# Kernel optimization log

Hardware: AMD Instinct MI355X
Metric: run time of the kernel (lower is better)

Reference implementation:

```python
import jax, jax.numpy as jnp
import numpy as np

F = 32  # node channels (both convs)


def ecc_conv(x, src, dst, e, fgn_w, fgn_b, root, bias):
    """Edge-conditioned conv: per-edge kernel from edge feats, gather-matmul-scatter."""
    n_nodes = x.shape[0]
    n_edges = e.shape[0]
    f_in = x.shape[1]
    # filter-generating network: (E, S) -> (E, F_in*F_out) -> (E, F_in, F_out)
    kernels = (e @ fgn_w + fgn_b).reshape(n_edges, f_in, F)
    # gather source node feats, per-edge matmul
    messages = jnp.einsum('ef,efo->eo', x[src], kernels)
    # scatter-sum to target nodes
    agg = jax.ops.segment_sum(messages, dst, num_segments=n_nodes)
    return jax.nn.relu(agg + x @ root + bias)


def setup_inputs() -> dict:
    key = jax.random.key(0)
    ks = jax.random.split(key, 12)
    N, E, S = 50000, 200000, 16
    s = 0.05  # small init scale to keep activations bounded through relu
    return {
        'x': jax.random.normal(ks[0], (N, F), jnp.float32),
        'e': jax.random.normal(ks[1], (E, S), jnp.float32),
        'src': jax.random.randint(ks[2], (E,), 0, N, jnp.int32),
        'dst': jax.random.randint(ks[3], (E,), 0, N, jnp.int32),
        'fgn_w1': jax.random.normal(ks[4], (S, F * F), jnp.float32) * s,
        'fgn_b1': jnp.zeros((F * F,), jnp.float32),
        'root1': jax.random.normal(ks[5], (F, F), jnp.float32) * s,
        'bias1': jnp.zeros((F,), jnp.float32),
        'fgn_w2': jax.random.normal(ks[6], (S, F * F), jnp.float32) * s,
        'fgn_b2': jnp.zeros((F * F,), jnp.float32),
        'root2': jax.random.normal(ks[7], (F, F), jnp.float32) * s,
        'bias2': jnp.zeros((F,), jnp.float32),
        'dense_w': jax.random.normal(ks[8], (F, 1), jnp.float32) * s,
        'dense_b': jnp.zeros((1,), jnp.float32),
    }


def reference(x, e, src, dst, fgn_w1, fgn_b1, root1, bias1,
              fgn_w2, fgn_b2, root2, bias2, dense_w, dense_b):
    h = ecc_conv(x, src, dst, e, fgn_w1, fgn_b1, root1, bias1)
    h = ecc_conv(h, src, dst, e, fgn_w2, fgn_b2, root2, bias2)
    pooled = jnp.sum(h, axis=0)          # global sum pool over nodes -> (F,)
    return pooled @ dense_w + dense_b    # (1,)
```

## Files before the change

kernel.cpp:

```cpp
#include <hip/hip_runtime.h>
#include <hip/hip_bf16.h>
#include <hip/hip_fp16.h>

#define F 32
#define S 16

typedef short v8s __attribute__((ext_vector_type(8)));
typedef _Float16 v8h __attribute__((ext_vector_type(8)));
typedef float v4f __attribute__((ext_vector_type(4)));

__device__ __forceinline__ float bf_lo(unsigned u) { return __uint_as_float(u << 16); }
__device__ __forceinline__ float bf_hi(unsigned u) { return __uint_as_float(u & 0xffff0000u); }
__device__ __forceinline__ unsigned short f2bf(float f) {
    __hip_bfloat16 h = __float2bfloat16(f);
    return *(unsigned short*)&h;
}
__device__ __forceinline__ unsigned short f2h(float f) {
    __half h = __float2half(f);
    return *(unsigned short*)&h;
}
__device__ __forceinline__ unsigned pack2(float a, float b) {
    __hip_bfloat162 h2 = __float22bfloat162_rn(make_float2(a, b));
    return *(unsigned*)&h2;
}
__device__ __forceinline__ unsigned pack2h(float a, float b) {
    __half2 h2 = __floats2half2_rn(a, b);
    return *(unsigned*)&h2;
}
static inline size_t align256(size_t b) { return (b + 255) & ~(size_t)255; }

__global__ __launch_bounds__(256) void prep_kernel(
    const float* __restrict__ w1, const float* __restrict__ b1, const float* __restrict__ r1,
    const float* __restrict__ w2, const float* __restrict__ b2, const float* __restrict__ r2,
    unsigned short* __restrict__ Wf1, unsigned short* __restrict__ Wf2,
    unsigned short* __restrict__ Rt1, unsigned short* __restrict__ Rt2,
    const int* __restrict__ dst, int* __restrict__ cnt,
    const float* __restrict__ x, unsigned short* __restrict__ x16,
    int N, int E, int eB)
{
    const int PER = 34 * 512 + 32 * 32;
    if (blockIdx.x < 144) {
        int tid = blockIdx.x * blockDim.x + threadIdx.x;
        if (tid >= 2 * PER) return;
        const int layer = tid / PER;
        const int rem   = tid % PER;
        const float* w = layer ? w2 : w1;
        const float* b = layer ? b2 : b1;
        const float* r = layer ? r2 : r1;
        if (rem < 34 * 512) {
            const int fi   = rem >> 9;
            const int rr   = rem & 511;
            const int lane = rr >> 3;
            const int j    = rr & 7;
            const int half = fi & 1;
            const int ck   = fi >> 1;
            const int o    = (half << 4) | (lane & 15);
            const int k    = ck * 32 + (lane >> 4) * 8 + j;
            const int s    = k >> 5, f = k & 31;
            const float v  = (s < S) ? w[s * (F * F) + f * F + o] : b[f * F + o];
            (layer ? Wf2 : Wf1)[rem] = f2h(v);
        } else {
            const int q = rem - 34 * 512;
            const int o = q >> 5, f = q & 31;
            (layer ? Rt2 : Rt1)[o * F + f] = f2bf(r[f * F + o]);
        }
    } else if (blockIdx.x < 144 + eB) {
        const int e = (blockIdx.x - 144) * blockDim.x + threadIdx.x;
        if (e < E) atomicAdd(&cnt[dst[e]], 1);
    } else {
        const int idx = (blockIdx.x - 144 - eB) * 256 + threadIdx.x;
        if (idx < N * 4) {
            const float4* p = (const float4*)(x + (size_t)idx * 8);
            float4 a = p[0], b = p[1];
            uint4 o;
            o.x = pack2h(a.x, a.y); o.y = pack2h(a.z, a.w);
            o.z = pack2h(b.x, b.y); o.w = pack2h(b.z, b.w);
            *(uint4*)(x16 + (size_t)idx * 8) = o;
        }
    }
}

__global__ __launch_bounds__(256) void scan_partial(
    const int* __restrict__ cnt, int* __restrict__ partial, int N)
{
    const int i = blockIdx.x * 256 + threadIdx.x;
    int v = (i < N) ? cnt[i] : 0;
    #pragma unroll
    for (int off = 32; off > 0; off >>= 1) v += __shfl_down(v, off, 64);
    __shared__ int wsum[4];
    const int wave = threadIdx.x >> 6, lane = threadIdx.x & 63;
    if (lane == 0) wsum[wave] = v;
    __syncthreads();
    if (threadIdx.x == 0)
        partial[blockIdx.x] = wsum[0] + wsum[1] + wsum[2] + wsum[3];
}

__global__ __launch_bounds__(256) void scan_final(
    const int* __restrict__ cnt, const int* __restrict__ partial,
    int* __restrict__ cursor, int* __restrict__ rowptr, int N)
{
    const int tid = threadIdx.x;
    __shared__ int pacc[256];
    int pre = 0;
    for (int j = tid; j < blockIdx.x; j += 256) pre += partial[j];
    pacc[tid] = pre;
    __syncthreads();
    #pragma unroll
    for (int off = 128; off > 0; off >>= 1) {
        if (tid < off) pacc[tid] += pacc[tid + off];
        __syncthreads();
    }
    const int blockPre = pacc[0];

    const int i = blockIdx.x * 256 + tid;
    const int v0 = (i < N) ? cnt[i] : 0;
    int v = v0;
    const int wave = tid >> 6, lane = tid & 63;
    #pragma unroll
    for (int off = 1; off < 64; off <<= 1) {
        int u = __shfl_up(v, off, 64);
        if (lane >= off) v += u;
    }
    __shared__ int wsum[4];
    if (lane == 63) wsum[wave] = v;
    __syncthreads();
    int woff = 0;
    for (int ww = 0; ww < 4; ++ww) woff += (ww < wave) ? wsum[ww] : 0;
    if (i < N) {
        const int excl = blockPre + woff + (v - v0);
        cursor[i] = excl;
        rowptr[i] = excl;
    }
}

__global__ __launch_bounds__(256) void scatter_kernel(
    const int* __restrict__ dst, int* __restrict__ cursor,
    int* __restrict__ perm, int E)
{
    int e = blockIdx.x * blockDim.x + threadIdx.x;
    if (e < E) {
        int p = atomicAdd(&cursor[dst[e]], 1);
        perm[p] = e;
    }
}

__global__ __launch_bounds__(256) void edge_msg(
    const unsigned short* __restrict__ x16,
    const float* __restrict__ ef,
    const int* __restrict__ src,
    const unsigned short* __restrict__ Wf,
    unsigned short* __restrict__ msg,
    int E)
{
    __shared__ v8h Wl[34 * 64];
    const int tid  = threadIdx.x;
    const int w    = tid >> 6;
    const int lane = tid & 63;
    const int lid  = lane & 15;
    const int quad = lane >> 4;

    {
        const uint4* s = (const uint4*)Wf;
        uint4* d = (uint4*)Wl;
        #pragma unroll
        for (int i = 0; i < 9; ++i) {
            const int idx = tid + 256 * i;
            if (idx < 2176) d[idx] = s[idx];
        }
    }
    __syncthreads();

    const int nTiles = (E + 15) >> 4;
    const int stride = gridDim.x * 4;
    int tile = blockIdx.x * 4 + w;
    if (tile >= nTiles) return;

    int  slot = tile * 16 + lid;
    bool live = (slot < E);
    int  s0   = live ? slot : 0;
    int  sn   = src[s0];
    v8h xh = *(const v8h*)(x16 + (size_t)sn * F + quad * 8);
    const float4* efv = (const float4*)(ef + (size_t)s0 * S);
    float4 c0 = efv[0], c1 = efv[1], c2 = efv[2], c3 = efv[3];

    while (true) {
        const int nextTile = tile + stride;
        v8h nxh;
        float4 nc0, nc1, nc2, nc3;
        bool nlive = false;
        if (nextTile < nTiles) {
            const int  ns_  = nextTile * 16 + lid;
            nlive = (ns_ < E);
            const int  ns0_ = nlive ? ns_ : 0;
            const int  nsn  = src[ns0_];
            nxh = *(const v8h*)(x16 + (size_t)nsn * F + quad * 8);
            const float4* nefv = (const float4*)(ef + (size_t)ns0_ * S);
            nc0 = nefv[0]; nc1 = nefv[1]; nc2 = nefv[2]; nc3 = nefv[3];
        }

        const float cs[S] = {c0.x, c0.y, c0.z, c0.w, c1.x, c1.y, c1.z, c1.w,
                             c2.x, c2.y, c2.z, c2.w, c3.x, c3.y, c3.z, c3.w};

        union { v8h h8; __half2 h2[4]; } xu;
        xu.h8 = xh;

        v4f acc0 = {0.f, 0.f, 0.f, 0.f};
        v4f acc1 = {0.f, 0.f, 0.f, 0.f};

        #pragma unroll
        for (int ck = 0; ck < S; ++ck) {
            const __half2 cc = __floats2half2_rn(cs[ck], cs[ck]);
            union { v8h h8; __half2 h2[4]; } fr;
            fr.h2[0] = __hmul2(cc, xu.h2[0]);
            fr.h2[1] = __hmul2(cc, xu.h2[1]);
            fr.h2[2] = __hmul2(cc, xu.h2[2]);
            fr.h2[3] = __hmul2(cc, xu.h2[3]);
            acc0 = __builtin_amdgcn_mfma_f32_16x16x32_f16(Wl[(2 * ck) * 64 + lane],     fr.h8, acc0, 0, 0, 0);
            acc1 = __builtin_amdgcn_mfma_f32_16x16x32_f16(Wl[(2 * ck + 1) * 64 + lane], fr.h8, acc1, 0, 0, 0);
        }
        acc0 = __builtin_amdgcn_mfma_f32_16x16x32_f16(Wl[32 * 64 + lane], xu.h8, acc0, 0, 0, 0);
        acc1 = __builtin_amdgcn_mfma_f32_16x16x32_f16(Wl[33 * 64 + lane], xu.h8, acc1, 0, 0, 0);

        if (live) {
            unsigned short* mp = msg + (size_t)slot * 32;
            uint2 p0, p1;
            p0.x = pack2(acc0[0], acc0[1]);
            p0.y = pack2(acc0[2], acc0[3]);
            p1.x = pack2(acc1[0], acc1[1]);
            p1.y = pack2(acc1[2], acc1[3]);
            *(uint2*)(mp + quad * 4)      = p0;
            *(uint2*)(mp + 16 + quad * 4) = p1;
        }

        if (nextTile >= nTiles) break;
        tile = nextTile;
        slot = tile * 16 + lid;
        live = nlive;
        xh = nxh;
        c0 = nc0; c1 = nc1; c2 = nc2; c3 = nc3;
    }
}

__global__ __launch_bounds__(256) void rootsum(
    const float* __restrict__ in,
    const unsigned short* __restrict__ msg,
    const int* __restrict__ rowptr,
    const int* __restrict__ cnt,
    const int* __restrict__ perm,
    const unsigned short* __restrict__ Rt,
    const float* __restrict__ bias,
    unsigned short* __restrict__ h16,
    int N)
{
    __shared__ float acc[64 * 33];
    __shared__ unsigned short As[64 * F];
    const int tid  = threadIdx.x;
    const int n0   = blockIdx.x * 64;
    const int w    = tid >> 6;
    const int lane = tid & 63;
    const int lid  = lane & 15;
    const int quad = lane >> 4;

    {
        const int nl = tid >> 2;
        const int kq = tid & 3;
        int n = n0 + nl; if (n > N - 1) n = N - 1;
        const float4* xp = (const float4*)(in + (size_t)n * F + kq * 8);
        float4 v0 = xp[0], v1 = xp[1];
        uint4 pk;
        pk.x = pack2(v0.x, v0.y);
        pk.y = pack2(v0.z, v0.w);
        pk.z = pack2(v1.x, v1.y);
        pk.w = pack2(v1.z, v1.w);
        const int slot = ((nl >> 4) * 4 + kq) * 16 + (nl & 15);
        *(uint4*)(As + slot * 8) = pk;
    }

    {
        const int nl = tid >> 2;
        const int oq = tid & 3;
        const int n  = n0 + nl;
        float a[8];
        #pragma unroll
        for (int j = 0; j < 8; ++j) a[j] = 0.f;
        if (n < N) {
            const int k0 = rowptr[n];
            const int k1 = k0 + cnt[n];
            for (int k = k0; k < k1; ++k) {
                const int e = perm[k];
                const uint4 q = *(const uint4*)(msg + (size_t)e * 32 + oq * 8);
                a[0] += bf_lo(q.x); a[1] += bf_hi(q.x);
                a[2] += bf_lo(q.y); a[3] += bf_hi(q.y);
                a[4] += bf_lo(q.z); a[5] += bf_hi(q.z);
                a[6] += bf_lo(q.w); a[7] += bf_hi(q.w);
            }
        }
        float* ap = acc + nl * 33 + oq * 8;
        #pragma unroll
        for (int j = 0; j < 8; ++j) ap[j] = a[j];
    }
    __syncthreads();

    const int jt  = w & 1;
    const int ns0 = (w >> 1) * 2;
    const v8s rf = *(const v8s*)(Rt + (size_t)(jt * 16 + lid) * F + quad * 8);
    const int o0 = jt * 16 + quad * 4;
    const float4 bs = *(const float4*)(bias + o0);

    #pragma unroll
    for (int i = 0; i < 2; ++i) {
        const int ns = ns0 + i;
        const v8s af = *(const v8s*)(As + (((ns * 4 + quad) * 16) + lid) * 8);
        v4f d = {0.f, 0.f, 0.f, 0.f};
        d = __builtin_amdgcn_mfma_f32_16x16x32_bf16(rf, af, d, 0, 0, 0);
        const int n = n0 + ns * 16 + lid;
        if (n < N) {
            const float* ap = acc + (ns * 16 + lid) * 33 + o0;
            float4 hv;
            hv.x = fmaxf(d[0] + ap[0] + bs.x, 0.f);
            hv.y = fmaxf(d[1] + ap[1] + bs.y, 0.f);
            hv.z = fmaxf(d[2] + ap[2] + bs.z, 0.f);
            hv.w = fmaxf(d[3] + ap[3] + bs.w, 0.f);
            uint2 hp;
            hp.x = pack2h(hv.x, hv.y);
            hp.y = pack2h(hv.z, hv.w);
            *(uint2*)(h16 + (size_t)n * F + o0) = hp;
        }
    }
}

__global__ __launch_bounds__(256) void rootsum_pool(
    const unsigned short* __restrict__ in16,
    const unsigned short* __restrict__ msg,
    const int* __restrict__ rowptr,
    const int* __restrict__ cnt,
    const int* __restrict__ perm,
    const unsigned short* __restrict__ Rt,
    const float* __restrict__ bias,
    float* __restrict__ bs,
    int N)
{
    __shared__ float acc[64 * 33];
    __shared__ unsigned short As[64 * F];
    __shared__ float poolbuf[4][16];
    const int tid  = threadIdx.x;
    const int n0   = blockIdx.x * 64;
    const int w    = tid >> 6;
    const int lane = tid & 63;
    const int lid  = lane & 15;
    const int quad = lane >> 4;

    {
        const int nl = tid >> 2;
        const int kq = tid & 3;
        int n = n0 + nl; if (n > N - 1) n = N - 1;
        const uint4 hv4 = *(const uint4*)(in16 + (size_t)n * F + kq * 8);
        const __half2* hh = (const __half2*)&hv4;
        float2 f0 = __half22float2(hh[0]);
        float2 f1 = __half22float2(hh[1]);
        float2 f2 = __half22float2(hh[2]);
        float2 f3 = __half22float2(hh[3]);
        uint4 pk;
        pk.x = pack2(f0.x, f0.y);
        pk.y = pack2(f1.x, f1.y);
        pk.z = pack2(f2.x, f2.y);
        pk.w = pack2(f3.x, f3.y);
        const int slot = ((nl >> 4) * 4 + kq) * 16 + (nl & 15);
        *(uint4*)(As + slot * 8) = pk;
    }

    {
        const int nl = tid >> 2;
        const int oq = tid & 3;
        const int n  = n0 + nl;
        float a[8];
        #pragma unroll
        for (int j = 0; j < 8; ++j) a[j] = 0.f;
        if (n < N) {
            const int k0 = rowptr[n];
            const int k1 = k0 + cnt[n];
            for (int k = k0; k < k1; ++k) {
                const int e = perm[k];
                const uint4 q = *(const uint4*)(msg + (size_t)e * 32 + oq * 8);
                a[0] += bf_lo(q.x); a[1] += bf_hi(q.x);
                a[2] += bf_lo(q.y); a[3] += bf_hi(q.y);
                a[4] += bf_lo(q.z); a[5] += bf_hi(q.z);
                a[6] += bf_lo(q.w); a[7] += bf_hi(q.w);
            }
        }
        float* ap = acc + nl * 33 + oq * 8;
        #pragma unroll
        for (int j = 0; j < 8; ++j) ap[j] = a[j];
    }
    __syncthreads();

    const int jt  = w & 1;
    const int ns0 = (w >> 1) * 2;
    const v8s rf = *(const v8s*)(Rt + (size_t)(jt * 16 + lid) * F + quad * 8);
    const int o0 = jt * 16 + quad * 4;
    const float4 bs4 = *(const float4*)(bias + o0);

    float psum[4] = {0.f, 0.f, 0.f, 0.f};

    #pragma unroll
    for (int i = 0; i < 2; ++i) {
        const int ns = ns0 + i;
        const v8s af = *(const v8s*)(As + (((ns * 4 + quad) * 16) + lid) * 8);
        v4f d = {0.f, 0.f, 0.f, 0.f};
        d = __builtin_amdgcn_mfma_f32_16x16x32_bf16(rf, af, d, 0, 0, 0);
        const int n = n0 + ns * 16 + lid;
        if (n < N) {
            const float* ap = acc + (ns * 16 + lid) * 33 + o0;
            psum[0] += fmaxf(d[0] + ap[0] + bs4.x, 0.f);
            psum[1] += fmaxf(d[1] + ap[1] + bs4.y, 0.f);
            psum[2] += fmaxf(d[2] + ap[2] + bs4.z, 0.f);
            psum[3] += fmaxf(d[3] + ap[3] + bs4.w, 0.f);
        }
    }

    #pragma unroll
    for (int m = 1; m < 16; m <<= 1) {
        psum[0] += __shfl_xor(psum[0], m, 64);
        psum[1] += __shfl_xor(psum[1], m, 64);
        psum[2] += __shfl_xor(psum[2], m, 64);
        psum[3] += __shfl_xor(psum[3], m, 64);
    }
    if (lid == 0) {
        #pragma unroll
        for (int j = 0; j < 4; ++j) poolbuf[w][quad * 4 + j] = psum[j];
    }
    __syncthreads();
    if (tid < 32) {
        const int jt2 = tid >> 4, idx = tid & 15;
        bs[(size_t)blockIdx.x * 32 + tid] = poolbuf[jt2][idx] + poolbuf[jt2 + 2][idx];
    }
}

__global__ __launch_bounds__(256) void final_fused(
    const float* __restrict__ bs, int nb,
    const float* __restrict__ dw, const float* __restrict__ db,
    float* __restrict__ out)
{
    const int ch = threadIdx.x & 31, g = threadIdx.x >> 5;
    float s = 0.f;
    for (int b = g; b < nb; b += 8) s += bs[(size_t)b * 32 + ch];
    __shared__ float red[256];
    red[threadIdx.x] = s;
    __syncthreads();
    if (threadIdx.x < 128) red[threadIdx.x] += red[threadIdx.x + 128];
    __syncthreads();
    if (threadIdx.x < 64) red[threadIdx.x] += red[threadIdx.x + 64];
    __syncthreads();
    if (threadIdx.x < 32) red[threadIdx.x] = (red[threadIdx.x] + red[threadIdx.x + 32]) * dw[threadIdx.x];
    __syncthreads();
    if (threadIdx.x == 0) {
        float t = 0.f;
        #pragma unroll
        for (int i = 0; i < 32; ++i) t += red[i];
        out[0] = t + db[0];
    }
}

__global__ __launch_bounds__(256) void pool_kernel(
    const float* __restrict__ h, float* __restrict__ pooled, int N)
{
    const int c = threadIdx.x & (F - 1);
    float p = 0.0f;
    for (int n = blockIdx.x * 8 + (threadIdx.x >> 5); n < N; n += gridDim.x * 8)
        p += h[(size_t)n * F + c];
    __shared__ float red[256];
    red[threadIdx.x] = p;
    __syncthreads();
    for (int off = 128; off >= F; off >>= 1) {
        if (threadIdx.x < off) red[threadIdx.x] += red[threadIdx.x + off];
        __syncthreads();
    }
    if (threadIdx.x < F) atomicAdd(&pooled[threadIdx.x], red[threadIdx.x]);
}

__global__ void final_kernel(
    const float* __restrict__ pooled, const float* __restrict__ dw,
    const float* __restrict__ db, float* __restrict__ out)
{
    const int o = threadIdx.x;
    float v = (o < F) ? pooled[o] * dw[o] : 0.0f;
    #pragma unroll
    for (int off = 32; off > 0; off >>= 1) v += __shfl_down(v, off, 64);
    if (o == 0) out[0] = v + db[0];
}

__global__ __launch_bounds__(256, 2) void ecc_edge_slow(
    const float* __restrict__ x, const float* __restrict__ ef,
    const int* __restrict__ src, const int* __restrict__ dst,
    const float* __restrict__ W, const float* __restrict__ B,
    float* __restrict__ agg, int E)
{
    const int tid = blockIdx.x * blockDim.x + threadIdx.x;
    const bool live = (tid < E);
    const int e = live ? tid : (E - 1);
    const int sn = src[e], dn = dst[e];
    float xr[F];
    const float4* xp = (const float4*)(x + (size_t)sn * F);
    #pragma unroll
    for (int i = 0; i < F / 4; ++i) {
        float4 v = xp[i];
        xr[4*i+0] = v.x; xr[4*i+1] = v.y; xr[4*i+2] = v.z; xr[4*i+3] = v.w;
    }
    float acc[F];
    #pragma unroll
    for (int o = 0; o < F; ++o) acc[o] = 0.0f;
    const float* erow = ef + (size_t)e * S;
    for (int s = 0; s < S; ++s) {
        const float es = erow[s];
        const float* Ws = W + s * (F * F);
        #pragma unroll
        for (int f = 0; f < F; ++f) {
            const float z = es * xr[f];
            #pragma unroll
            for (int o = 0; o < F; ++o) acc[o] = fmaf(z, Ws[f * F + o], acc[o]);
        }
    }
    #pragma unroll
    for (int f = 0; f < F; ++f) {
        const float xf = xr[f];
        #pragma unroll
        for (int o = 0; o < F; ++o) acc[o] = fmaf(xf, B[f * F + o], acc[o]);
    }
    if (live) {
        float* ap = agg + (size_t)dn * F;
        #pragma unroll
        for (int o = 0; o < F; ++o) atomicAdd(ap + o, acc[o]);
    }
}

__global__ __launch_bounds__(256) void ecc_node_slow(
    const float* __restrict__ xin, const float* __restrict__ root,
    const float* __restrict__ bias, float* __restrict__ h, int N)
{
    int t = blockIdx.x * blockDim.x + threadIdx.x;
    if (t >= N * F) return;
    const int n = t >> 5, o = t & (F - 1);
    const float* xrow = xin + (size_t)n * F;
    float v = h[t] + bias[o];
    #pragma unroll
    for (int f = 0; f < F; ++f) v = fmaf(xrow[f], root[f * F + o], v);
    h[t] = fmaxf(v, 0.0f);
}

extern "C" void kernel_launch(void* const* d_in, const int* in_sizes, int n_in,
                              void* d_out, int out_size, void* d_ws, size_t ws_size,
                              hipStream_t stream) {
    const float* x      = (const float*)d_in[0];
    const float* efeat  = (const float*)d_in[1];
    const int*   src    = (const int*)d_in[2];
    const int*   dst    = (const int*)d_in[3];
    const float* fgn_w1 = (const float*)d_in[4];
    const float* fgn_b1 = (const float*)d_in[5];
    const float* root1  = (const float*)d_in[6];
    const float* bias1  = (const float*)d_in[7];
    const float* fgn_w2 = (const float*)d_in[8];
    const float* fgn_b2 = (const float*)d_in[9];
    const float* root2  = (const float*)d_in[10];
    const float* bias2  = (const float*)d_in[11];
    const float* dense_w = (const float*)d_in[12];
    const float* dense_b = (const float*)d_in[13];

    const int N = in_sizes[0] / F;
    const int E = in_sizes[2];

    const int gridP    = (N + 255) / 256;
    const int rsBlocks = (N + 63) / 64;

    const size_t pooledB = 256;
    const size_t cntB    = align256((size_t)N * 4);
    const size_t rowB    = align256((size_t)N * 4);
    const size_t curB    = align256((size_t)N * 4);
    const size_t partB   = align256((size_t)gridP * 4);
    const size_t permB   = align256((size_t)E * 4);
    const size_t efsB    = align256((size_t)E * S * 4);
    const size_t srcsB   = align256((size_t)E * 4);
    const size_t msgB    = align256((size_t)E * 32 * 2);
    const size_t hB      = (size_t)N * F * 4;
    const size_t wfB     = align256((size_t)34 * 512 * 2);
    const size_t rtB     = align256((size_t)32 * 32 * 2);
    const size_t x16B    = align256((size_t)N * F * 2);

    const size_t offCnt  = pooledB;
    const size_t offRow  = offCnt + cntB;
    const size_t offCur  = offRow + rowB;
    const size_t offPart = offCur + curB;
    const size_t offPerm = offPart + partB;
    const size_t offEfs  = offPerm + permB;
    const size_t offSrcs = offEfs + efsB;
    const size_t offMsg  = offSrcs + srcsB;
    const size_t offH1   = offMsg + msgB;
    const size_t offH2   = offH1 + hB;
    const size_t offW1   = offH2 + hB;
    const size_t offW2   = offW1 + wfB;
    const size_t offR1   = offW2 + wfB;
    const size_t offR2   = offR1 + rtB;
    const size_t need    = offR2 + rtB;

    const int eB         = (E + 255) / 256;
    const int nodeBlocks = (N * F + 255) / 256;

    if (ws_size >= need && efsB >= 2 * x16B) {
        int* cnt     = (int*)((char*)d_ws + offCnt);
        int* rowptr  = (int*)((char*)d_ws + offRow);
        int* cursor  = (int*)((char*)d_ws + offCur);
        int* partial = (int*)((char*)d_ws + offPart);
        int* perm    = (int*)((char*)d_ws + offPerm);
        unsigned short* x16 = (unsigned short*)((char*)d_ws + offEfs);
        unsigned short* h16 = (unsigned short*)((char*)d_ws + offEfs + x16B);
        unsigned short* msg = (unsigned short*)((char*)d_ws + offMsg);
        float* bsum  = (float*)((char*)d_ws + offH2);
        unsigned short* Wf1 = (unsigned short*)((char*)d_ws + offW1);
        unsigned short* Wf2 = (unsigned short*)((char*)d_ws + offW2);
        unsigned short* Rt1 = (unsigned short*)((char*)d_ws + offR1);
        unsigned short* Rt2 = (unsigned short*)((char*)d_ws + offR2);

        hipMemsetAsync(d_ws, 0, pooledB + cntB, stream);

        const int xcB = (N * 4 + 255) / 256;
        prep_kernel<<<144 + eB + xcB, 256, 0, stream>>>(
            fgn_w1, fgn_b1, root1, fgn_w2, fgn_b2, root2,
            Wf1, Wf2, Rt1, Rt2, dst, cnt, x, x16, N, E, eB);

        scan_partial  <<<gridP, 256, 0, stream>>>(cnt, partial, N);
        scan_final    <<<gridP, 256, 0, stream>>>(cnt, partial, cursor, rowptr, N);
        scatter_kernel<<<eB, 256, 0, stream>>>(dst, cursor, perm, E);

        const int nTiles = (E + 15) / 16;
        int edgeBlocks = (nTiles + 3) / 4;
        if (edgeBlocks > 1024) edgeBlocks = 1024;

        edge_msg<<<edgeBlocks, 256, 0, stream>>>(x16, efeat, src, Wf1, msg, E);
        rootsum <<<rsBlocks, 256, 0, stream>>>(x, msg, rowptr, cnt, perm, Rt1, bias1, h16, N);

        edge_msg    <<<edgeBlocks, 256, 0, stream>>>(h16, efeat, src, Wf2, msg, E);
        rootsum_pool<<<rsBlocks, 256, 0, stream>>>(h16, msg, rowptr, cnt, perm, Rt2, bias2, bsum, N);

        final_fused<<<1, 256, 0, stream>>>(bsum, rsBlocks, dense_w, dense_b, (float*)d_out);
    } else {
        float* agg1   = (float*)d_ws;
        float* agg2   = agg1 + (size_t)N * F;
        float* pooled = agg2 + (size_t)N * F;
        hipMemsetAsync(d_ws, 0, (2 * (size_t)N * F + F) * sizeof(float), stream);
        ecc_edge_slow<<<eB, 256, 0, stream>>>(x, efeat, src, dst, fgn_w1, fgn_b1, agg1, E);
        ecc_node_slow<<<nodeBlocks, 256, 0, stream>>>(x, root1, bias1, agg1, N);
        ecc_edge_slow<<<eB, 256, 0, stream>>>(agg1, efeat, src, dst, fgn_w2, fgn_b2, agg2, E);
        ecc_node_slow<<<nodeBlocks, 256, 0, stream>>>(agg1, root2, bias2, agg2, N);
        pool_kernel <<<512, 256, 0, stream>>>(agg2, pooled, N);
        final_kernel<<<1, 64, 0, stream>>>(pooled, dense_w, dense_b, (float*)d_out);
    }
}
```

Baseline: 192.8 us.

## Write edge messages directly in destination-sorted order via inverse permutation

The scatter kernel now records, for each edge, its position in the destination-sorted order, and edge_msg writes each message straight to that sorted slot. The rootsum kernels then read messages contiguously by CSR index, which drops the perm indirection and the random 64-byte gathers. In exchange the message writes from edge_msg become scattered rather than coalesced, and each edge tile does one extra index load.

```diff
diff --git a/kernel.cpp b/kernel.cpp
--- a/kernel.cpp
+++ b/kernel.cpp
@@ -135,12 +135,12 @@
 
 __global__ __launch_bounds__(256) void scatter_kernel(
     const int* __restrict__ dst, int* __restrict__ cursor,
-    int* __restrict__ perm, int E)
+    int* __restrict__ inv, int E)
 {
     int e = blockIdx.x * blockDim.x + threadIdx.x;
     if (e < E) {
         int p = atomicAdd(&cursor[dst[e]], 1);
-        perm[p] = e;
+        inv[e] = p;
     }
 }
 
@@ -148,6 +148,7 @@
     const unsigned short* __restrict__ x16,
     const float* __restrict__ ef,
     const int* __restrict__ src,
+    const int* __restrict__ inv,
     const unsigned short* __restrict__ Wf,
     unsigned short* __restrict__ msg,
     int E)
@@ -179,6 +180,7 @@
     bool live = (slot < E);
     int  s0   = live ? slot : 0;
     int  sn   = src[s0];
+    int  iv   = inv[s0];
     v8h xh = *(const v8h*)(x16 + (size_t)sn * F + quad * 8);
     const float4* efv = (const float4*)(ef + (size_t)s0 * S);
     float4 c0 = efv[0], c1 = efv[1], c2 = efv[2], c3 = efv[3];
@@ -187,12 +189,14 @@
         const int nextTile = tile + stride;
         v8h nxh;
         float4 nc0, nc1, nc2, nc3;
+        int niv = 0;
         bool nlive = false;
         if (nextTile < nTiles) {
             const int  ns_  = nextTile * 16 + lid;
             nlive = (ns_ < E);
             const int  ns0_ = nlive ? ns_ : 0;
             const int  nsn  = src[ns0_];
+            niv = inv[ns0_];
             nxh = *(const v8h*)(x16 + (size_t)nsn * F + quad * 8);
             const float4* nefv = (const float4*)(ef + (size_t)ns0_ * S);
             nc0 = nefv[0]; nc1 = nefv[1]; nc2 = nefv[2]; nc3 = nefv[3];
@@ -222,7 +226,7 @@
         acc1 = __builtin_amdgcn_mfma_f32_16x16x32_f16(Wl[33 * 64 + lane], xu.h8, acc1, 0, 0, 0);
 
         if (live) {
-            unsigned short* mp = msg + (size_t)slot * 32;
+            unsigned short* mp = msg + (size_t)iv * 32;
             uint2 p0, p1;
             p0.x = pack2(acc0[0], acc0[1]);
             p0.y = pack2(acc0[2], acc0[3]);
@@ -237,6 +241,7 @@
         slot = tile * 16 + lid;
         live = nlive;
         xh = nxh;
+        iv = niv;
         c0 = nc0; c1 = nc1; c2 = nc2; c3 = nc3;
     }
 }
@@ -246,7 +251,6 @@
     const unsigned short* __restrict__ msg,
     const int* __restrict__ rowptr,
     const int* __restrict__ cnt,
-    const int* __restrict__ perm,
     const unsigned short* __restrict__ Rt,
     const float* __restrict__ bias,
     unsigned short* __restrict__ h16,
@@ -287,8 +291,7 @@
             const int k0 = rowptr[n];
             const int k1 = k0 + cnt[n];
             for (int k = k0; k < k1; ++k) {
-                const int e = perm[k];
-                const uint4 q = *(const uint4*)(msg + (size_t)e * 32 + oq * 8);
+                const uint4 q = *(const uint4*)(msg + (size_t)k * 32 + oq * 8);
                 a[0] += bf_lo(q.x); a[1] += bf_hi(q.x);
                 a[2] += bf_lo(q.y); a[3] += bf_hi(q.y);
                 a[4] += bf_lo(q.z); a[5] += bf_hi(q.z);
@@ -334,7 +337,6 @@
     const unsigned short* __restrict__ msg,
     const int* __restrict__ rowptr,
     const int* __restrict__ cnt,
-    const int* __restrict__ perm,
     const unsigned short* __restrict__ Rt,
     const float* __restrict__ bias,
     float* __restrict__ bs,
@@ -380,8 +382,7 @@
             const int k0 = rowptr[n];
             const int k1 = k0 + cnt[n];
             for (int k = k0; k < k1; ++k) {
-                const int e = perm[k];
-                const uint4 q = *(const uint4*)(msg + (size_t)e * 32 + oq * 8);
+                const uint4 q = *(const uint4*)(msg + (size_t)k * 32 + oq * 8);
                 a[0] += bf_lo(q.x); a[1] += bf_hi(q.x);
                 a[2] += bf_lo(q.y); a[3] += bf_hi(q.y);
                 a[4] += bf_lo(q.z); a[5] += bf_hi(q.z);
@@ -609,7 +610,7 @@
         int* rowptr  = (int*)((char*)d_ws + offRow);
         int* cursor  = (int*)((char*)d_ws + offCur);
         int* partial = (int*)((char*)d_ws + offPart);
-        int* perm    = (int*)((char*)d_ws + offPerm);
+        int* inv     = (int*)((char*)d_ws + offPerm);
         unsigned short* x16 = (unsigned short*)((char*)d_ws + offEfs);
         unsigned short* h16 = (unsigned short*)((char*)d_ws + offEfs + x16B);
         unsigned short* msg = (unsigned short*)((char*)d_ws + offMsg);
@@ -628,17 +629,17 @@
 
         scan_partial  <<<gridP, 256, 0, stream>>>(cnt, partial, N);
         scan_final    <<<gridP, 256, 0, stream>>>(cnt, partial, cursor, rowptr, N);
-        scatter_kernel<<<eB, 256, 0, stream>>>(dst, cursor, perm, E);
+        scatter_kernel<<<eB, 256, 0, stream>>>(dst, cursor, inv, E);
 
         const int nTiles = (E + 15) / 16;
         int edgeBlocks = (nTiles + 3) / 4;
         if (edgeBlocks > 1024) edgeBlocks = 1024;
 
-        edge_msg<<<edgeBlocks, 256, 0, stream>>>(x16, efeat, src, Wf1, msg, E);
-        rootsum <<<rsBlocks, 256, 0, stream>>>(x, msg, rowptr, cnt, perm, Rt1, bias1, h16, N);
-
-        edge_msg    <<<edgeBlocks, 256, 0, stream>>>(h16, efeat, src, Wf2, msg, E);
-        rootsum_pool<<<rsBlocks, 256, 0, stream>>>(h16, msg, rowptr, cnt, perm, Rt2, bias2, bsum, N);
+        edge_msg<<<edgeBlocks, 256, 0, stream>>>(x16, efeat, src, inv, Wf1, msg, E);
+        rootsum <<<rsBlocks, 256, 0, stream>>>(x, msg, rowptr, cnt, Rt1, bias1, h16, N);
+
+        edge_msg    <<<edgeBlocks, 256, 0, stream>>>(h16, efeat, src, inv, Wf2, msg, E);
+        rootsum_pool<<<rsBlocks, 256, 0, stream>>>(h16, msg, rowptr, cnt, Rt2, bias2, bsum, N);
 
         final_fused<<<1, 256, 0, stream>>>(bsum, rsBlocks, dense_w, dense_b, (float*)d_out);
     } else {
```

Result: faster. 184.9 us, median of 2 (-4.1%).

## Fuse per-edge message compute with destination-sorted aggregation per node block

Applied to the files above, without the earlier changes.

Merges the edge message kernel and the node root/sum kernel into one kernel per layer. Each block owns 64 destination nodes and walks their CSR-sorted edges, computing messages with MFMA and accumulating into shared memory via LDS atomics after a binary search over row pointers. This removes the bf16 message buffer write and re-read and two launches. In exchange each block reloads the filter weights, edge gathers now go through perm (less coalesced), shared-memory atomics add contention, and blocks with many edges may cause load imbalance.

```diff
diff --git a/kernel.cpp b/kernel.cpp
--- a/kernel.cpp
+++ b/kernel.cpp
@@ -144,16 +144,24 @@
     }
 }
 
-__global__ __launch_bounds__(256) void edge_msg(
-    const unsigned short* __restrict__ x16,
+__global__ __launch_bounds__(256) void ecc_layer1(
+    const unsigned short* __restrict__ in16,
     const float* __restrict__ ef,
     const int* __restrict__ src,
+    const int* __restrict__ perm,
+    const int* __restrict__ rowptr,
     const unsigned short* __restrict__ Wf,
-    unsigned short* __restrict__ msg,
-    int E)
+    const unsigned short* __restrict__ Rt,
+    const float* __restrict__ bias,
+    unsigned short* __restrict__ h16,
+    int N, int E)
 {
     __shared__ v8h Wl[34 * 64];
+    __shared__ float acc[64 * 33];
+    __shared__ unsigned short As[64 * F];
+    __shared__ int rp[65];
     const int tid  = threadIdx.x;
+    const int n0   = blockIdx.x * 64;
     const int w    = tid >> 6;
     const int lane = tid & 63;
     const int lid  = lane & 15;
@@ -168,45 +176,67 @@
             if (idx < 2176) d[idx] = s[idx];
         }
     }
-    __syncthreads();
-
-    const int nTiles = (E + 15) >> 4;
-    const int stride = gridDim.x * 4;
-    int tile = blockIdx.x * 4 + w;
-    if (tile >= nTiles) return;
-
-    int  slot = tile * 16 + lid;
-    bool live = (slot < E);
-    int  s0   = live ? slot : 0;
-    int  sn   = src[s0];
-    v8h xh = *(const v8h*)(x16 + (size_t)sn * F + quad * 8);
-    const float4* efv = (const float4*)(ef + (size_t)s0 * S);
-    float4 c0 = efv[0], c1 = efv[1], c2 = efv[2], c3 = efv[3];
-
-    while (true) {
-        const int nextTile = tile + stride;
-        v8h nxh;
-        float4 nc0, nc1, nc2, nc3;
-        bool nlive = false;
-        if (nextTile < nTiles) {
-            const int  ns_  = nextTile * 16 + lid;
-            nlive = (ns_ < E);
-            const int  ns0_ = nlive ? ns_ : 0;
-            const int  nsn  = src[ns0_];
-            nxh = *(const v8h*)(x16 + (size_t)nsn * F + quad * 8);
-            const float4* nefv = (const float4*)(ef + (size_t)ns0_ * S);
-            nc0 = nefv[0]; nc1 = nefv[1]; nc2 = nefv[2]; nc3 = nefv[3];
+    for (int i = tid; i < 64 * 33; i += 256) acc[i] = 0.f;
+    if (tid < 65) {
+        const int n = n0 + tid;
+        rp[tid] = (n < N) ? rowptr[n] : E;
+    }
+    {
+        const int nl = tid >> 2;
+        const int kq = tid & 3;
+        int n = n0 + nl; if (n > N - 1) n = N - 1;
+        const uint4 hv4 = *(const uint4*)(in16 + (size_t)n * F + kq * 8);
+        const __half2* hh = (const __half2*)&hv4;
+        float2 f0 = __half22float2(hh[0]);
+        float2 f1 = __half22float2(hh[1]);
+        float2 f2 = __half22float2(hh[2]);
+        float2 f3 = __half22float2(hh[3]);
+        uint4 pk;
+        pk.x = pack2(f0.x, f0.y);
+        pk.y = pack2(f1.x, f1.y);
+        pk.z = pack2(f2.x, f2.y);
+        pk.w = pack2(f3.x, f3.y);
+        const int slot = ((nl >> 4) * 4 + kq) * 16 + (nl & 15);
+        *(uint4*)(As + slot * 8) = pk;
+    }
+    __syncthreads();
+
+    const int k0 = rp[0];
+    const int k1 = rp[64];
+
+    int t = k0 + w * 16;
+    v8h xh = {};
+    float4 c0{}, c1{}, c2{}, c3{};
+    if (t < k1) {
+        const int s_ = t + lid;
+        const int sl = (s_ < k1) ? s_ : k0;
+        const int e  = perm[sl];
+        const int sn = src[e];
+        xh = *(const v8h*)(in16 + (size_t)sn * F + quad * 8);
+        const float4* efv = (const float4*)(ef + (size_t)e * S);
+        c0 = efv[0]; c1 = efv[1]; c2 = efv[2]; c3 = efv[3];
+    }
+    while (t < k1) {
+        const int tn = t + 64;
+        v8h nxh = {};
+        float4 nc0{}, nc1{}, nc2{}, nc3{};
+        if (tn < k1) {
+            const int s_ = tn + lid;
+            const int sl = (s_ < k1) ? s_ : k0;
+            const int e  = perm[sl];
+            const int sn = src[e];
+            nxh = *(const v8h*)(in16 + (size_t)sn * F + quad * 8);
+            const float4* efv = (const float4*)(ef + (size_t)e * S);
+            nc0 = efv[0]; nc1 = efv[1]; nc2 = efv[2]; nc3 = efv[3];
         }
 
         const float cs[S] = {c0.x, c0.y, c0.z, c0.w, c1.x, c1.y, c1.z, c1.w,
                              c2.x, c2.y, c2.z, c2.w, c3.x, c3.y, c3.z, c3.w};
-
         union { v8h h8; __half2 h2[4]; } xu;
         xu.h8 = xh;
 
         v4f acc0 = {0.f, 0.f, 0.f, 0.f};
         v4f acc1 = {0.f, 0.f, 0.f, 0.f};
-
         #pragma unroll
         for (int ck = 0; ck < S; ++ck) {
             const __half2 cc = __floats2half2_rn(cs[ck], cs[ck]);
@@ -221,83 +251,25 @@
         acc0 = __builtin_amdgcn_mfma_f32_16x16x32_f16(Wl[32 * 64 + lane], xu.h8, acc0, 0, 0, 0);
         acc1 = __builtin_amdgcn_mfma_f32_16x16x32_f16(Wl[33 * 64 + lane], xu.h8, acc1, 0, 0, 0);
 
-        if (live) {
-            unsigned short* mp = msg + (size_t)slot * 32;
-            uint2 p0, p1;
-            p0.x = pack2(acc0[0], acc0[1]);
-            p0.y = pack2(acc0[2], acc0[3]);
-            p1.x = pack2(acc1[0], acc1[1]);
-            p1.y = pack2(acc1[2], acc1[3]);
-            *(uint2*)(mp + quad * 4)      = p0;
-            *(uint2*)(mp + 16 + quad * 4) = p1;
-        }
-
-        if (nextTile >= nTiles) break;
-        tile = nextTile;
-        slot = tile * 16 + lid;
-        live = nlive;
-        xh = nxh;
-        c0 = nc0; c1 = nc1; c2 = nc2; c3 = nc3;
-    }
-}
-
-__global__ __launch_bounds__(256) void rootsum(
-    const float* __restrict__ in,
-    const unsigned short* __restrict__ msg,
-    const int* __restrict__ rowptr,
-    const int* __restrict__ cnt,
-    const int* __restrict__ perm,
-    const unsigned short* __restrict__ Rt,
-    const float* __restrict__ bias,
-    unsigned short* __restrict__ h16,
-    int N)
-{
-    __shared__ float acc[64 * 33];
-    __shared__ unsigned short As[64 * F];
-    const int tid  = threadIdx.x;
-    const int n0   = blockIdx.x * 64;
-    const int w    = tid >> 6;
-    const int lane = tid & 63;
-    const int lid  = lane & 15;
-    const int quad = lane >> 4;
-
-    {
-        const int nl = tid >> 2;
-        const int kq = tid & 3;
-        int n = n0 + nl; if (n > N - 1) n = N - 1;
-        const float4* xp = (const float4*)(in + (size_t)n * F + kq * 8);
-        float4 v0 = xp[0], v1 = xp[1];
-        uint4 pk;
-        pk.x = pack2(v0.x, v0.y);
-        pk.y = pack2(v0.z, v0.w);
-        pk.z = pack2(v1.x, v1.y);
-        pk.w = pack2(v1.z, v1.w);
-        const int slot = ((nl >> 4) * 4 + kq) * 16 + (nl & 15);
-        *(uint4*)(As + slot * 8) = pk;
-    }
-
-    {
-        const int nl = tid >> 2;
-        const int oq = tid & 3;
-        const int n  = n0 + nl;
-        float a[8];
-        #pragma unroll
-        for (int j = 0; j < 8; ++j) a[j] = 0.f;
-        if (n < N) {
-            const int k0 = rowptr[n];
-            const int k1 = k0 + cnt[n];
-            for (int k = k0; k < k1; ++k) {
-                const int e = perm[k];
-                const uint4 q = *(const uint4*)(msg + (size_t)e * 32 + oq * 8);
-                a[0] += bf_lo(q.x); a[1] += bf_hi(q.x);
-                a[2] += bf_lo(q.y); a[3] += bf_hi(q.y);
-                a[4] += bf_lo(q.z); a[5] += bf_hi(q.z);
-                a[6] += bf_lo(q.w); a[7] += bf_hi(q.w);
+        {
+            const int s_ = t + lid;
+            if (s_ < k1) {
+                int lo = 0, hi = 63;
+                #pragma unroll
+                for (int it = 0; it < 6; ++it) {
+                    const int mid = (lo + hi + 1) >> 1;
+                    if (rp[mid] <= s_) lo = mid; else hi = mid - 1;
+                }
+                float* ap = acc + lo * 33;
+                #pragma unroll
+                for (int j = 0; j < 4; ++j) atomicAdd(ap + quad * 4 + j,      acc0[j]);
+                #pragma unroll
+                for (int j = 0; j < 4; ++j) atomicAdd(ap + 16 + quad * 4 + j, acc1[j]);
             }
         }
-        float* ap = acc + nl * 33 + oq * 8;
-        #pragma unroll
-        for (int j = 0; j < 8; ++j) ap[j] = a[j];
+
+        t = tn;
+        xh = nxh; c0 = nc0; c1 = nc1; c2 = nc2; c3 = nc3;
     }
     __syncthreads();
 
@@ -329,19 +301,22 @@
     }
 }
 
-__global__ __launch_bounds__(256) void rootsum_pool(
+__global__ __launch_bounds__(256) void ecc_layer2(
     const unsigned short* __restrict__ in16,
-    const unsigned short* __restrict__ msg,
+    const float* __restrict__ ef,
+    const int* __restrict__ src,
+    const int* __restrict__ perm,
     const int* __restrict__ rowptr,
-    const int* __restrict__ cnt,
-    const int* __restrict__ perm,
+    const unsigned short* __restrict__ Wf,
     const unsigned short* __restrict__ Rt,
     const float* __restrict__ bias,
-    float* __restrict__ bs,
-    int N)
-{
+    float* __restrict__ bsOut,
+    int N, int E)
+{
+    __shared__ v8h Wl[34 * 64];
     __shared__ float acc[64 * 33];
     __shared__ unsigned short As[64 * F];
+    __shared__ int rp[65];
     __shared__ float poolbuf[4][16];
     const int tid  = threadIdx.x;
     const int n0   = blockIdx.x * 64;
@@ -350,6 +325,20 @@
     const int lid  = lane & 15;
     const int quad = lane >> 4;
 
+    {
+        const uint4* s = (const uint4*)Wf;
+        uint4* d = (uint4*)Wl;
+        #pragma unroll
+        for (int i = 0; i < 9; ++i) {
+            const int idx = tid + 256 * i;
+            if (idx < 2176) d[idx] = s[idx];
+        }
+    }
+    for (int i = tid; i < 64 * 33; i += 256) acc[i] = 0.f;
+    if (tid < 65) {
+        const int n = n0 + tid;
+        rp[tid] = (n < N) ? rowptr[n] : E;
+    }
     {
         const int nl = tid >> 2;
         const int kq = tid & 3;
@@ -368,29 +357,77 @@
         const int slot = ((nl >> 4) * 4 + kq) * 16 + (nl & 15);
         *(uint4*)(As + slot * 8) = pk;
     }
-
-    {
-        const int nl = tid >> 2;
-        const int oq = tid & 3;
-        const int n  = n0 + nl;
-        float a[8];
-        #pragma unroll
-        for (int j = 0; j < 8; ++j) a[j] = 0.f;
-        if (n < N) {
-            const int k0 = rowptr[n];
-            const int k1 = k0 + cnt[n];
-            for (int k = k0; k < k1; ++k) {
-                const int e = perm[k];
-                const uint4 q = *(const uint4*)(msg + (size_t)e * 32 + oq * 8);
-                a[0] += bf_lo(q.x); a[1] += bf_hi(q.x);
-                a[2] += bf_lo(q.y); a[3] += bf_hi(q.y);
-                a[4] += bf_lo(q.z); a[5] += bf_hi(q.z);
-                a[6] += bf_lo(q.w); a[7] += bf_hi(q.w);
+    __syncthreads();
+
+    const int k0 = rp[0];
+    const int k1 = rp[64];
+
+    int t = k0 + w * 16;
+    v8h xh = {};
+    float4 c0{}, c1{}, c2{}, c3{};
+    if (t < k1) {
+        const int s_ = t + lid;
+        const int sl = (s_ < k1) ? s_ : k0;
+        const int e  = perm[sl];
+        const int sn = src[e];
+        xh = *(const v8h*)(in16 + (size_t)sn * F + quad * 8);
+        const float4* efv = (const float4*)(ef + (size_t)e * S);
+        c0 = efv[0]; c1 = efv[1]; c2 = efv[2]; c3 = efv[3];
+    }
+    while (t < k1) {
+        const int tn = t + 64;
+        v8h nxh = {};
+        float4 nc0{}, nc1{}, nc2{}, nc3{};
+        if (tn < k1) {
+            const int s_ = tn + lid;
+            const int sl = (s_ < k1) ? s_ : k0;
+            const int e  = perm[sl];
+            const int sn = src[e];
+            nxh = *(const v8h*)(in16 + (size_t)sn * F + quad * 8);
+            const float4* efv = (const float4*)(ef + (size_t)e * S);
+            nc0 = efv[0]; nc1 = efv[1]; nc2 = efv[2]; nc3 = efv[3];
+        }
+
+        const float cs[S] = {c0.x, c0.y, c0.z, c0.w, c1.x, c1.y, c1.z, c1.w,
+                             c2.x, c2.y, c2.z, c2.w, c3.x, c3.y, c3.z, c3.w};
+        union { v8h h8; __half2 h2[4]; } xu;
+        xu.h8 = xh;
+
+        v4f acc0 = {0.f, 0.f, 0.f, 0.f};
+        v4f acc1 = {0.f, 0.f, 0.f, 0.f};
+        #pragma unroll
+        for (int ck = 0; ck < S; ++ck) {
+            const __half2 cc = __floats2half2_rn(cs[ck], cs[ck]);
+            union { v8h h8; __half2 h2[4]; } fr;
+            fr.h2[0] = __hmul2(cc, xu.h2[0]);
+            fr.h2[1] = __hmul2(cc, xu.h2[1]);
+            fr.h2[2] = __hmul2(cc, xu.h2[2]);
+            fr.h2[3] = __hmul2(cc, xu.h2[3]);
+            acc0 = __builtin_amdgcn_mfma_f32_16x16x32_f16(Wl[(2 * ck) * 64 + lane],     fr.h8, acc0, 0, 0, 0);
+            acc1 = __builtin_amdgcn_mfma_f32_16x16x32_f16(Wl[(2 * ck + 1) * 64 + lane], fr.h8, acc1, 0, 0, 0);
+        }
+        acc0 = __builtin_amdgcn_mfma_f32_16x16x32_f16(Wl[32 * 64 + lane], xu.h8, acc0, 0, 0, 0);
+        acc1 = __builtin_amdgcn_mfma_f32_16x16x32_f16(Wl[33 * 64 + lane], xu.h8, acc1, 0, 0, 0);
+
+        {
+            const int s_ = t + lid;
+            if (s_ < k1) {
+                int lo = 0, hi = 63;
+                #pragma unroll
+                for (int it = 0; it < 6; ++it) {
+                    const int mid = (lo + hi + 1) >> 1;
+                    if (rp[mid] <= s_) lo = mid; else hi = mid - 1;
+                }
+                float* ap = acc + lo * 33;
+                #pragma unroll
+                for (int j = 0; j < 4; ++j) atomicAdd(ap + quad * 4 + j,      acc0[j]);
+                #pragma unroll
+                for (int j = 0; j < 4; ++j) atomicAdd(ap + 16 + quad * 4 + j, acc1[j]);
             }
         }
-        float* ap = acc + nl * 33 + oq * 8;
-        #pragma unroll
-        for (int j = 0; j < 8; ++j) ap[j] = a[j];
+
+        t = tn;
+        xh = nxh; c0 = nc0; c1 = nc1; c2 = nc2; c3 = nc3;
     }
     __syncthreads();
 
@@ -401,7 +438,6 @@
     const float4 bs4 = *(const float4*)(bias + o0);
 
     float psum[4] = {0.f, 0.f, 0.f, 0.f};
-
     #pragma unroll
     for (int i = 0; i < 2; ++i) {
         const int ns = ns0 + i;
@@ -432,7 +468,7 @@
     __syncthreads();
     if (tid < 32) {
         const int jt2 = tid >> 4, idx = tid & 15;
-        bs[(size_t)blockIdx.x * 32 + tid] = poolbuf[jt2][idx] + poolbuf[jt2 + 2][idx];
+        bsOut[(size_t)blockIdx.x * 32 + tid] = poolbuf[jt2][idx] + poolbuf[jt2 + 2][idx];
     }
 }
 
@@ -612,7 +648,6 @@
         int* perm    = (int*)((char*)d_ws + offPerm);
         unsigned short* x16 = (unsigned short*)((char*)d_ws + offEfs);
         unsigned short* h16 = (unsigned short*)((char*)d_ws + offEfs + x16B);
-        unsigned short* msg = (unsigned short*)((char*)d_ws + offMsg);
         float* bsum  = (float*)((char*)d_ws + offH2);
         unsigned short* Wf1 = (unsigned short*)((char*)d_ws + offW1);
         unsigned short* Wf2 = (unsigned short*)((char*)d_ws + offW2);
@@ -630,15 +665,10 @@
         scan_final    <<<gridP, 256, 0, stream>>>(cnt, partial, cursor, rowptr, N);
         scatter_kernel<<<eB, 256, 0, stream>>>(dst, cursor, perm, E);
 
-        const int nTiles = (E + 15) / 16;
-        int edgeBlocks = (nTiles + 3) / 4;
-        if (edgeBlocks > 1024) edgeBlocks = 1024;
-
-        edge_msg<<<edgeBlocks, 256, 0, stream>>>(x16, efeat, src, Wf1, msg, E);
-        rootsum <<<rsBlocks, 256, 0, stream>>>(x, msg, rowptr, cnt, perm, Rt1, bias1, h16, N);
-
-        edge_msg    <<<edgeBlocks, 256, 0, stream>>>(h16, efeat, src, Wf2, msg, E);
-        rootsum_pool<<<rsBlocks, 256, 0, stream>>>(h16, msg, rowptr, cnt, perm, Rt2, bias2, bsum, N);
+        ecc_layer1<<<rsBlocks, 256, 0, stream>>>(
+            x16, efeat, src, perm, rowptr, Wf1, Rt1, bias1, h16, N, E);
+        ecc_layer2<<<rsBlocks, 256, 0, stream>>>(
+            h16, efeat, src, perm, rowptr, Wf2, Rt2, bias2, bsum, N, E);
 
         final_fused<<<1, 256, 0, stream>>>(bsum, rsBlocks, dense_w, dense_b, (float*)d_out);
     } else {
```

Measured after the change: 275.0 us. 1.43x slower.
